# Kernel optimization log

Hardware: AMD Instinct MI355X
Metric: run time of the kernel (lower is better)

Reference implementation:

```python
import jax, jax.numpy as jnp
import numpy as np

LN_EPS = 1e-5


def setup_inputs() -> dict:
    key = jax.random.key(0)
    k1, k2, k3, k4, k5 = jax.random.split(key, 5)
    N, D, E, T = 100000, 128, 400000, 4  # nodes, feat dim, edges per etype, n etypes
    feat = jax.random.normal(k1, (N, D), dtype=jnp.float32)
    W = jax.random.normal(k2, (T, D, D), dtype=jnp.float32)
    Wf = jax.random.normal(k3, (T, D, 2 * D), dtype=jnp.float32)
    ln_w = jnp.ones((D,), dtype=jnp.float32)
    ln_b = jnp.zeros((D,), dtype=jnp.float32)
    src = jax.random.randint(k4, (T, E), 0, N, dtype=jnp.int32)
    dst = jax.random.randint(k5, (T, E), 0, N, dtype=jnp.int32)
    return {"feat": feat, "W": W, "Wf": Wf, "ln_w": ln_w, "ln_b": ln_b, "src": src, "dst": dst}


def reference(feat, W, Wf, ln_w, ln_b, src, dst):
    N, D = feat.shape
    T = W.shape[0]
    h = jnp.zeros((N, D), dtype=feat.dtype)
    for t in range(T):  # small fixed loop over edge types (structurally distinct weights)
        msg = feat @ W[t]                    # [N, D] per-src-node projection
        fw = feat @ Wf[t]                    # [N, 2D] FiLM params (dst ntype == src ntype)
        gamma, beta = fw[:, :D], fw[:, D:]
        m = jax.nn.relu(gamma * msg + beta)  # node-wise FiLM + ReLU, pre-scatter
        # copy_u -> gather message at edge src; fn.sum -> segment-sum into dst
        h = h + jax.ops.segment_sum(m[src[t]], dst[t], num_segments=N)
    # LayerNorm (elementwise affine); dropout omitted (eval mode)
    mu = jnp.mean(h, axis=-1, keepdims=True)
    var = jnp.mean(jnp.square(h - mu), axis=-1, keepdims=True)
    out = (h - mu) * jax.lax.rsqrt(var + LN_EPS) * ln_w + ln_b
    return out
```

## Files before the change

### kernel.cpp

```cpp
#include <hip/hip_runtime.h>
#include <hip/hip_bf16.h>

#define DD 128
#define LN_EPS 1e-5f
#define BCAP 3072
#define MAXBIN 1024
#define CHUNK 4096

typedef __bf16 bf16x8 __attribute__((ext_vector_type(8)));
typedef float f32x4 __attribute__((ext_vector_type(4)));

__device__ __forceinline__ float bflo(unsigned int u) { return __uint_as_float(u << 16); }
__device__ __forceinline__ float bfhi(unsigned int u) { return __uint_as_float(u & 0xffff0000u); }

__device__ __forceinline__ void gload_lds16(const void* g, void* lds) {
    __builtin_amdgcn_global_load_lds(
        (const __attribute__((address_space(1))) unsigned int*)g,
        (__attribute__((address_space(3))) unsigned int*)lds, 16, 0, 0);
}

__global__ __launch_bounds__(256) void k_pack_feat(const float* __restrict__ f,
                                                   unsigned short* __restrict__ fb, int n8) {
    int i = blockIdx.x * 256 + threadIdx.x;
    if (i >= n8) return;
    const float4* p = (const float4*)f + (size_t)i * 2;
    float4 v0 = p[0], v1 = p[1];
    float vv[8] = {v0.x, v0.y, v0.z, v0.w, v1.x, v1.y, v1.z, v1.w};
    unsigned short u[8];
#pragma unroll
    for (int j = 0; j < 8; j++) {
        __hip_bfloat16 b = __float2bfloat16(vv[j]);
        u[j] = *reinterpret_cast<unsigned short*>(&b);
    }
    uint4 o;
    o.x = u[0] | ((unsigned)u[1] << 16);
    o.y = u[2] | ((unsigned)u[3] << 16);
    o.z = u[4] | ((unsigned)u[5] << 16);
    o.w = u[6] | ((unsigned)u[7] << 16);
    ((uint4*)fb)[i] = o;
}

__global__ __launch_bounds__(256) void k_pack_w(const float* __restrict__ W,
                                                const float* __restrict__ Wf,
                                                unsigned short* __restrict__ wcat) {
    int i = blockIdx.x * 256 + threadIdx.x;
    if (i >= 4 * 384 * 128) return;
    int t = i / (384 * 128);
    int r = i % (384 * 128);
    int c = r / 128, k = r % 128;
    float v = (c < 128) ? W[((size_t)t * 128 + k) * 128 + c]
                        : Wf[((size_t)t * 128 + k) * 256 + (c - 128)];
    __hip_bfloat16 b = __float2bfloat16(v);
    wcat[i] = *reinterpret_cast<unsigned short*>(&b);
}

__global__ __launch_bounds__(256) void k_hist2(const int* __restrict__ dst,
                                               int* __restrict__ H, int E4, int NBLK, int NBIN) {
    __shared__ int h[MAXBIN];
    const int b = blockIdx.x;
    for (int j = threadIdx.x; j < NBIN; j += 256) h[j] = 0;
    __syncthreads();
    int base = b * CHUNK;
    int end = base + CHUNK < E4 ? base + CHUNK : E4;
    for (int i = base + threadIdx.x; i < end; i += 256) atomicAdd(&h[dst[i] >> 7], 1);
    __syncthreads();
    for (int j = threadIdx.x; j < NBIN; j += 256) H[(size_t)j * NBLK + b] = h[j];
}

__global__ __launch_bounds__(256) void k_scanbin(int* __restrict__ H, int* __restrict__ C,
                                                 int NBLK, int NBIN) {
    const int wv = (blockIdx.x * 256 + threadIdx.x) >> 6;
    const int lane = threadIdx.x & 63;
    if (wv >= NBIN) return;
    int* row = H + (size_t)wv * NBLK;
    int run = 0;
    for (int base = 0; base < NBLK; base += 64) {
        int idx = base + lane;
        int v = (idx < NBLK) ? row[idx] : 0;
        int s = v;
#pragma unroll
        for (int o = 1; o < 64; o <<= 1) {
            int u = __shfl_up(s, o, 64);
            if (lane >= o) s += u;
        }
        if (idx < NBLK) row[idx] = run + s - v;
        run += __shfl(s, 63, 64);
    }
    if (lane == 0) C[wv] = run;
}

__global__ __launch_bounds__(1024) void k_scan(const int* __restrict__ cnt,
                                               int* __restrict__ off, int NB) {
    __shared__ int s[1024];
    int tid = threadIdx.x;
    s[tid] = (tid < NB) ? cnt[tid] : 0;
    __syncthreads();
    for (int st = 1; st < 1024; st <<= 1) {
        int t = s[tid];
        int a = (tid >= st) ? s[tid - st] : 0;
        __syncthreads();
        s[tid] = t + a;
        __syncthreads();
    }
    if (tid < NB) {
        off[tid] = s[tid] - cnt[tid];
        if (tid == NB - 1) off[NB] = s[tid];
    }
}

__global__ __launch_bounds__(256) void k_place2(const int* __restrict__ src,
                                                const int* __restrict__ dst,
                                                const int* __restrict__ H,
                                                const int* __restrict__ binoff,
                                                unsigned int* __restrict__ rec,
                                                int N, int E, int E4, int NBLK, int NBIN) {
    __shared__ int fill[MAXBIN];
    const int b = blockIdx.x;
    for (int j = threadIdx.x; j < NBIN; j += 256)
        fill[j] = binoff[j] + H[(size_t)j * NBLK + b];
    __syncthreads();
    int base = b * CHUNK;
    int end = base + CHUNK < E4 ? base + CHUNK : E4;
    for (int i = base + threadIdx.x; i < end; i += 256) {
        int d = dst[i];
        int t = i / E;
        unsigned int r = ((unsigned)(d & 127) << 19) | (unsigned)(t * N + src[i]);
        int pos = atomicAdd(&fill[d >> 7], 1);
        rec[pos] = r;
    }
}

__global__ __launch_bounds__(256) void k_sortout(const unsigned int* __restrict__ rec,
                                                 const int* __restrict__ binoff,
                                                 unsigned int* __restrict__ sortedg,
                                                 int* __restrict__ nodestart,
                                                 int* __restrict__ nodedeg, int N) {
    __shared__ int lcnt[128], soff[128], sfill[128], tmp[128];
    __shared__ unsigned int sorted[BCAP];
    const int b = blockIdx.x, tid = threadIdx.x;
    const int s0 = binoff[b];
    int n = binoff[b + 1] - s0;
    if (n > BCAP) n = BCAP;

    if (tid < 128) lcnt[tid] = 0;
    __syncthreads();
    for (int j = tid; j < n; j += 256) atomicAdd(&lcnt[rec[s0 + j] >> 19], 1);
    __syncthreads();
    if (tid < 128) tmp[tid] = lcnt[tid];
    __syncthreads();
    for (int st = 1; st < 128; st <<= 1) {
        int t = 0, a = 0;
        if (tid < 128) {
            t = tmp[tid];
            a = (tid >= st) ? tmp[tid - st] : 0;
        }
        __syncthreads();
        if (tid < 128) tmp[tid] = t + a;
        __syncthreads();
    }
    if (tid < 128) {
        int ex = tmp[tid] - lcnt[tid];
        soff[tid] = ex;
        sfill[tid] = ex;
    }
    __syncthreads();
    for (int j = tid; j < n; j += 256) {
        unsigned int r = rec[s0 + j];
        int p = atomicAdd(&sfill[r >> 19], 1);
        sorted[p] = r & 0x7FFFFu;
    }
    __syncthreads();
    for (int j = tid; j < n; j += 256) sortedg[s0 + j] = sorted[j];
    if (tid < 128) {
        int node = b * 128 + tid;
        if (node < N) {
            nodestart[node] = s0 + soff[tid];
            nodedeg[node] = lcnt[tid];
        }
    }
}

__global__ __launch_bounds__(256, 2) void k_gemm_film(const unsigned short* __restrict__ featb,
                                                      const unsigned short* __restrict__ wcat,
                                                      unsigned short* __restrict__ m, int N,
                                                      int NT) {
    __shared__ unsigned char smem[2 * 16384];
    const int t = blockIdx.y;
    const int tid = threadIdx.x;
    const int w = tid >> 6, lane = tid & 63;
    const int lr = lane & 15, kg = lane >> 4;
    const int cbase = w * 32;

    const unsigned short* wt = wcat + (size_t)t * 384 * 128;
    bf16x8 B[4][3][2];
#pragma unroll
    for (int kkI = 0; kkI < 4; kkI++)
#pragma unroll
        for (int mat = 0; mat < 3; mat++)
#pragma unroll
            for (int cj = 0; cj < 2; cj++) {
                int col = mat * 128 + cbase + cj * 16 + lr;
                B[kkI][mat][cj] = *(const bf16x8*)(wt + (size_t)col * 128 + kkI * 32 + kg * 8);
            }

    auto stage = [&](int buf, int r0) {
#pragma unroll
        for (int it = 0; it < 4; it++) {
            int row = it * 16 + w * 4 + (lane >> 4);
            int gr = r0 + row;
            if (gr >= N) gr = N - 1;
            int x = ((lane & 15) * 16) ^ ((row & 7) << 4);
            const unsigned char* g = (const unsigned char*)featb + (size_t)gr * 256 + x;
            gload_lds16(g, smem + buf * 16384 + it * 4096 + w * 1024);
        }
    };

    unsigned short* mt = m + (size_t)t * N * DD;
    int buf = 0;
    int tile = blockIdx.x;
    if (tile < NT) stage(0, tile * 64);

    for (; tile < NT; tile += gridDim.x) {
        __syncthreads();
        int nxt = tile + gridDim.x;
        if (nxt < NT) stage(buf ^ 1, nxt * 64);

        const unsigned char* sm = smem + buf * 16384;
        f32x4 acc[4][3][2] = {};
#pragma unroll
        for (int kkI = 0; kkI < 4; kkI++) {
            bf16x8 a[4];
#pragma unroll
            for (int mi = 0; mi < 4; mi++) {
                int row = mi * 16 + lr;
                int kb = kkI * 64 + kg * 16;
                a[mi] = *(const bf16x8*)(sm + row * 256 + (kb ^ ((row & 7) << 4)));
            }
#pragma unroll
            for (int mi = 0; mi < 4; mi++)
#pragma unroll
                for (int mat = 0; mat < 3; mat++)
#pragma unroll
                    for (int cj = 0; cj < 2; cj++)
                        acc[mi][mat][cj] = __builtin_amdgcn_mfma_f32_16x16x32_bf16(
                            a[mi], B[kkI][mat][cj], acc[mi][mat][cj], 0, 0, 0);
        }

        const int r0 = tile * 64;
#pragma unroll
        for (int mi = 0; mi < 4; mi++)
#pragma unroll
            for (int cj = 0; cj < 2; cj++)
#pragma unroll
                for (int r = 0; r < 4; r++) {
                    int row = r0 + mi * 16 + kg * 4 + r;
                    if (row < N) {
                        float v = acc[mi][1][cj][r] * acc[mi][0][cj][r] + acc[mi][2][cj][r];
                        v = fmaxf(v, 0.0f);
                        __hip_bfloat16 b = __float2bfloat16(v);
                        mt[(size_t)row * DD + cbase + cj * 16 + lr] =
                            *reinterpret_cast<unsigned short*>(&b);
                    }
                }
        buf ^= 1;
    }
}

__global__ __launch_bounds__(256) void k_agg_ln(const unsigned int* __restrict__ sortedg,
                                                const int* __restrict__ nodestart,
                                                const int* __restrict__ nodedeg,
                                                const char* __restrict__ mbase,
                                                const float* __restrict__ lnw,
                                                const float* __restrict__ lnb,
                                                float* __restrict__ out, int N) {
    const int wv = threadIdx.x >> 6, lane = threadIdx.x & 63;
    const int node = blockIdx.x * 4 + wv;
    if (node >= N) return;
    const int start = nodestart[node], deg = nodedeg[node];
    const int q = lane >> 4, sl = lane & 15;
    const unsigned soff = (unsigned)sl * 16u;

    float a[8] = {0.f, 0.f, 0.f, 0.f, 0.f, 0.f, 0.f, 0.f};

    int e = 0;
    for (; e + 16 <= deg; e += 16) {
        unsigned r0 = sortedg[start + e + q];
        unsigned r1 = sortedg[start + e + 4 + q];
        unsigned r2 = sortedg[start + e + 8 + q];
        unsigned r3 = sortedg[start + e + 12 + q];
        uint4 p0 = *(const uint4*)(mbase + (r0 * 256u + soff));
        uint4 p1 = *(const uint4*)(mbase + (r1 * 256u + soff));
        uint4 p2 = *(const uint4*)(mbase + (r2 * 256u + soff));
        uint4 p3 = *(const uint4*)(mbase + (r3 * 256u + soff));
        a[0] += bflo(p0.x) + bflo(p1.x) + bflo(p2.x) + bflo(p3.x);
        a[1] += bfhi(p0.x) + bfhi(p1.x) + bfhi(p2.x) + bfhi(p3.x);
        a[2] += bflo(p0.y) + bflo(p1.y) + bflo(p2.y) + bflo(p3.y);
        a[3] += bfhi(p0.y) + bfhi(p1.y) + bfhi(p2.y) + bfhi(p3.y);
        a[4] += bflo(p0.z) + bflo(p1.z) + bflo(p2.z) + bflo(p3.z);
        a[5] += bfhi(p0.z) + bfhi(p1.z) + bfhi(p2.z) + bfhi(p3.z);
        a[6] += bflo(p0.w) + bflo(p1.w) + bflo(p2.w) + bflo(p3.w);
        a[7] += bfhi(p0.w) + bfhi(p1.w) + bfhi(p2.w) + bfhi(p3.w);
    }
    for (; e + 4 <= deg; e += 4) {
        unsigned r0 = sortedg[start + e + q];
        uint4 p0 = *(const uint4*)(mbase + (r0 * 256u + soff));
        a[0] += bflo(p0.x);
        a[1] += bfhi(p0.x);
        a[2] += bflo(p0.y);
        a[3] += bfhi(p0.y);
        a[4] += bflo(p0.z);
        a[5] += bfhi(p0.z);
        a[6] += bflo(p0.w);
        a[7] += bfhi(p0.w);
    }
    if (e < deg) {
        int idx = e + q;
        float w = (idx < deg) ? 1.0f : 0.0f;
        if (idx >= deg) idx = deg - 1;
        unsigned r0 = sortedg[start + idx];
        uint4 p0 = *(const uint4*)(mbase + (r0 * 256u + soff));
        a[0] += w * bflo(p0.x);
        a[1] += w * bfhi(p0.x);
        a[2] += w * bflo(p0.y);
        a[3] += w * bfhi(p0.y);
        a[4] += w * bflo(p0.z);
        a[5] += w * bfhi(p0.z);
        a[6] += w * bflo(p0.w);
        a[7] += w * bfhi(p0.w);
    }

#pragma unroll
    for (int j = 0; j < 8; j++) {
        a[j] += __shfl_xor(a[j], 16, 64);
        a[j] += __shfl_xor(a[j], 32, 64);
    }
    float s = 0.f, ss = 0.f;
#pragma unroll
    for (int j = 0; j < 8; j++) {
        s += a[j];
        ss += a[j] * a[j];
    }
#pragma unroll
    for (int o = 1; o < 16; o <<= 1) {
        s += __shfl_xor(s, o, 64);
        ss += __shfl_xor(ss, o, 64);
    }
    float mu = s * (1.0f / 128.0f);
    float var = ss * (1.0f / 128.0f) - mu * mu;
    float rstd = rsqrtf(var + LN_EPS);
    if (q == 0) {
        float4 w0 = ((const float4*)lnw)[sl * 2];
        float4 w1 = ((const float4*)lnw)[sl * 2 + 1];
        float4 b0 = ((const float4*)lnb)[sl * 2];
        float4 b1 = ((const float4*)lnb)[sl * 2 + 1];
        float4 o0, o1;
        o0.x = (a[0] - mu) * rstd * w0.x + b0.x;
        o0.y = (a[1] - mu) * rstd * w0.y + b0.y;
        o0.z = (a[2] - mu) * rstd * w0.z + b0.z;
        o0.w = (a[3] - mu) * rstd * w0.w + b0.w;
        o1.x = (a[4] - mu) * rstd * w1.x + b1.x;
        o1.y = (a[5] - mu) * rstd * w1.y + b1.y;
        o1.z = (a[6] - mu) * rstd * w1.z + b1.z;
        o1.w = (a[7] - mu) * rstd * w1.w + b1.w;
        ((float4*)(out + (size_t)node * DD))[sl * 2] = o0;
        ((float4*)(out + (size_t)node * DD))[sl * 2 + 1] = o1;
    }
}

extern "C" void kernel_launch(void* const* d_in, const int* in_sizes, int n_in,
                              void* d_out, int out_size, void* d_ws, size_t ws_size,
                              hipStream_t stream) {
    const float* feat = (const float*)d_in[0];
    const float* W    = (const float*)d_in[1];
    const float* Wf   = (const float*)d_in[2];
    const float* lnw  = (const float*)d_in[3];
    const float* lnb  = (const float*)d_in[4];
    const int* src    = (const int*)d_in[5];
    const int* dst    = (const int*)d_in[6];
    float* out = (float*)d_out;

    const int N = in_sizes[0] / DD;
    const int E = in_sizes[5] / 4;
    const int E4 = 4 * E;
    const int NB = (N + 127) >> 7;
    const int NBLK = (E4 + CHUNK - 1) / CHUNK;
    const int NT = (N + 63) / 64;

    size_t off = 0;
    char* ws = (char*)d_ws;
    auto alloc = [&](size_t bytes) -> void* {
        void* p = ws + off;
        off += (bytes + 255) & ~(size_t)255;
        return p;
    };
    unsigned short* m     = (unsigned short*)alloc((size_t)4 * N * DD * 2);
    unsigned short* featb = (unsigned short*)alloc((size_t)N * DD * 2);
    unsigned short* wcat  = (unsigned short*)alloc((size_t)4 * 384 * 128 * 2);
    int* H      = (int*)alloc((size_t)NB * NBLK * 4);
    int* C      = (int*)alloc((size_t)NB * 4);
    int* binoff = (int*)alloc((size_t)(NB + 1) * 4);
    unsigned int* rec     = (unsigned int*)alloc((size_t)E4 * 4);
    unsigned int* sortedg = (unsigned int*)alloc((size_t)E4 * 4);
    int* nodestart = (int*)alloc((size_t)N * 4);
    int* nodedeg   = (int*)alloc((size_t)N * 4);
    if (off > ws_size) return;

    int n8 = N * DD / 8;
    k_pack_feat<<<(n8 + 255) / 256, 256, 0, stream>>>(feat, featb, n8);
    k_pack_w<<<(4 * 384 * 128 + 255) / 256, 256, 0, stream>>>(W, Wf, wcat);
    k_hist2<<<NBLK, 256, 0, stream>>>(dst, H, E4, NBLK, NB);
    k_scanbin<<<(NB * 64 + 255) / 256, 256, 0, stream>>>(H, C, NBLK, NB);
    k_scan<<<1, 1024, 0, stream>>>(C, binoff, NB);
    k_place2<<<NBLK, 256, 0, stream>>>(src, dst, H, binoff, rec, N, E, E4, NBLK, NB);
    k_sortout<<<NB, 256, 0, stream>>>(rec, binoff, sortedg, nodestart, nodedeg, N);
    dim3 gg(128, 4);
    k_gemm_film<<<gg, 256, 0, stream>>>(featb, wcat, m, N, NT);
    k_agg_ln<<<(N + 3) / 4, 256, 0, stream>>>(sortedg, nodestart, nodedeg,
                                              (const char*)m, lnw, lnb, out, N);
}
```

Baseline: 173.2 us.

## Fuse preprocessing and bucket-sort kernels into one cooperative kernel with grid syncs

Merges the feature and weight bf16 packing, histogram, bin scan, global scan, placement and per-bin sort into a single cooperative kernel. Grid-wide syncs separate the phases instead of seven separate launches, and the sort phase uses a grid-stride loop over bins. This removes launch overhead and inter-kernel gaps. The risk is that the grid (NBLK of about 391 blocks at 256 threads, 14KB LDS each) must be fully co-resident for the cooperative launch, and grid.sync itself has a cost.

```diff
diff --git a/kernel.cpp b/kernel.cpp
--- a/kernel.cpp
+++ b/kernel.cpp
@@ -1,5 +1,8 @@
 #include <hip/hip_runtime.h>
 #include <hip/hip_bf16.h>
+#include <hip/hip_cooperative_groups.h>
+
+namespace cg = cooperative_groups;
 
 #define DD 128
 #define LN_EPS 1e-5f
@@ -19,163 +22,182 @@
         (__attribute__((address_space(3))) unsigned int*)lds, 16, 0, 0);
 }
 
-__global__ __launch_bounds__(256) void k_pack_feat(const float* __restrict__ f,
-                                                   unsigned short* __restrict__ fb, int n8) {
-    int i = blockIdx.x * 256 + threadIdx.x;
-    if (i >= n8) return;
-    const float4* p = (const float4*)f + (size_t)i * 2;
-    float4 v0 = p[0], v1 = p[1];
-    float vv[8] = {v0.x, v0.y, v0.z, v0.w, v1.x, v1.y, v1.z, v1.w};
-    unsigned short u[8];
-#pragma unroll
-    for (int j = 0; j < 8; j++) {
-        __hip_bfloat16 b = __float2bfloat16(vv[j]);
-        u[j] = *reinterpret_cast<unsigned short*>(&b);
-    }
-    uint4 o;
-    o.x = u[0] | ((unsigned)u[1] << 16);
-    o.y = u[2] | ((unsigned)u[3] << 16);
-    o.z = u[4] | ((unsigned)u[5] << 16);
-    o.w = u[6] | ((unsigned)u[7] << 16);
-    ((uint4*)fb)[i] = o;
-}
-
-__global__ __launch_bounds__(256) void k_pack_w(const float* __restrict__ W,
-                                                const float* __restrict__ Wf,
-                                                unsigned short* __restrict__ wcat) {
-    int i = blockIdx.x * 256 + threadIdx.x;
-    if (i >= 4 * 384 * 128) return;
-    int t = i / (384 * 128);
-    int r = i % (384 * 128);
-    int c = r / 128, k = r % 128;
-    float v = (c < 128) ? W[((size_t)t * 128 + k) * 128 + c]
-                        : Wf[((size_t)t * 128 + k) * 256 + (c - 128)];
-    __hip_bfloat16 b = __float2bfloat16(v);
-    wcat[i] = *reinterpret_cast<unsigned short*>(&b);
-}
-
-__global__ __launch_bounds__(256) void k_hist2(const int* __restrict__ dst,
-                                               int* __restrict__ H, int E4, int NBLK, int NBIN) {
-    __shared__ int h[MAXBIN];
-    const int b = blockIdx.x;
-    for (int j = threadIdx.x; j < NBIN; j += 256) h[j] = 0;
+__global__ __launch_bounds__(256) void k_prep(const float* __restrict__ feat,
+                                              const float* __restrict__ W,
+                                              const float* __restrict__ Wf,
+                                              const int* __restrict__ src,
+                                              const int* __restrict__ dst,
+                                              unsigned short* __restrict__ fb,
+                                              unsigned short* __restrict__ wcat,
+                                              int* __restrict__ H, int* __restrict__ C,
+                                              int* __restrict__ binoff,
+                                              unsigned int* __restrict__ rec,
+                                              unsigned int* __restrict__ sortedg,
+                                              int* __restrict__ nodestart,
+                                              int* __restrict__ nodedeg,
+                                              int N, int E, int E4, int NBLK, int NBIN,
+                                              int n8) {
+    cg::grid_group grid = cg::this_grid();
+    __shared__ int shm[3584];
+    const int b = blockIdx.x, tid = threadIdx.x;
+    const int gtid = b * 256 + tid, gsz = gridDim.x * 256;
+
+    for (int j = tid; j < NBIN; j += 256) shm[j] = 0;
     __syncthreads();
-    int base = b * CHUNK;
-    int end = base + CHUNK < E4 ? base + CHUNK : E4;
-    for (int i = base + threadIdx.x; i < end; i += 256) atomicAdd(&h[dst[i] >> 7], 1);
+    {
+        int base = b * CHUNK;
+        int end = base + CHUNK < E4 ? base + CHUNK : E4;
+        for (int i = base + tid; i < end; i += 256) atomicAdd(&shm[dst[i] >> 7], 1);
+    }
     __syncthreads();
-    for (int j = threadIdx.x; j < NBIN; j += 256) H[(size_t)j * NBLK + b] = h[j];
-}
-
-__global__ __launch_bounds__(256) void k_scanbin(int* __restrict__ H, int* __restrict__ C,
-                                                 int NBLK, int NBIN) {
-    const int wv = (blockIdx.x * 256 + threadIdx.x) >> 6;
-    const int lane = threadIdx.x & 63;
-    if (wv >= NBIN) return;
-    int* row = H + (size_t)wv * NBLK;
-    int run = 0;
-    for (int base = 0; base < NBLK; base += 64) {
-        int idx = base + lane;
-        int v = (idx < NBLK) ? row[idx] : 0;
-        int s = v;
-#pragma unroll
-        for (int o = 1; o < 64; o <<= 1) {
-            int u = __shfl_up(s, o, 64);
-            if (lane >= o) s += u;
-        }
-        if (idx < NBLK) row[idx] = run + s - v;
-        run += __shfl(s, 63, 64);
-    }
-    if (lane == 0) C[wv] = run;
-}
-
-__global__ __launch_bounds__(1024) void k_scan(const int* __restrict__ cnt,
-                                               int* __restrict__ off, int NB) {
-    __shared__ int s[1024];
-    int tid = threadIdx.x;
-    s[tid] = (tid < NB) ? cnt[tid] : 0;
+    for (int j = tid; j < NBIN; j += 256) H[(size_t)j * NBLK + b] = shm[j];
+
+    for (int i = gtid; i < n8; i += gsz) {
+        const float4* p = (const float4*)feat + (size_t)i * 2;
+        float4 v0 = p[0], v1 = p[1];
+        float vv[8] = {v0.x, v0.y, v0.z, v0.w, v1.x, v1.y, v1.z, v1.w};
+        unsigned short u[8];
+#pragma unroll
+        for (int j = 0; j < 8; j++) {
+            __hip_bfloat16 bb = __float2bfloat16(vv[j]);
+            u[j] = *reinterpret_cast<unsigned short*>(&bb);
+        }
+        uint4 o;
+        o.x = u[0] | ((unsigned)u[1] << 16);
+        o.y = u[2] | ((unsigned)u[3] << 16);
+        o.z = u[4] | ((unsigned)u[5] << 16);
+        o.w = u[6] | ((unsigned)u[7] << 16);
+        ((uint4*)fb)[i] = o;
+    }
+
+    for (int i = gtid; i < 4 * 384 * 128; i += gsz) {
+        int t = i / (384 * 128);
+        int r = i % (384 * 128);
+        int c = r / 128, k = r % 128;
+        float v = (c < 128) ? W[((size_t)t * 128 + k) * 128 + c]
+                            : Wf[((size_t)t * 128 + k) * 256 + (c - 128)];
+        __hip_bfloat16 bb = __float2bfloat16(v);
+        wcat[i] = *reinterpret_cast<unsigned short*>(&bb);
+    }
+
+    grid.sync();
+
+    {
+        int wv = gtid >> 6;
+        int lane = tid & 63;
+        if (wv < NBIN) {
+            int* row = H + (size_t)wv * NBLK;
+            int run = 0;
+            for (int base = 0; base < NBLK; base += 64) {
+                int idx = base + lane;
+                int v = (idx < NBLK) ? row[idx] : 0;
+                int s = v;
+#pragma unroll
+                for (int o = 1; o < 64; o <<= 1) {
+                    int u = __shfl_up(s, o, 64);
+                    if (lane >= o) s += u;
+                }
+                if (idx < NBLK) row[idx] = run + s - v;
+                run += __shfl(s, 63, 64);
+            }
+            if (lane == 0) C[wv] = run;
+        }
+    }
+
+    grid.sync();
+
+    if (b == 0) {
+        int v[4];
+        int tot = 0;
+#pragma unroll
+        for (int j = 0; j < 4; j++) {
+            int idx = tid * 4 + j;
+            v[j] = (idx < NBIN) ? C[idx] : 0;
+            tot += v[j];
+        }
+        shm[tid] = tot;
+        __syncthreads();
+        for (int st = 1; st < 256; st <<= 1) {
+            int t = shm[tid];
+            int add = (tid >= st) ? shm[tid - st] : 0;
+            __syncthreads();
+            shm[tid] = t + add;
+            __syncthreads();
+        }
+        int run = shm[tid] - tot;
+#pragma unroll
+        for (int j = 0; j < 4; j++) {
+            int idx = tid * 4 + j;
+            if (idx < NBIN) binoff[idx] = run;
+            run += v[j];
+        }
+        if (tid == 255) binoff[NBIN] = shm[255];
+    }
+
+    grid.sync();
+
+    for (int j = tid; j < NBIN; j += 256) shm[j] = binoff[j] + H[(size_t)j * NBLK + b];
     __syncthreads();
-    for (int st = 1; st < 1024; st <<= 1) {
-        int t = s[tid];
-        int a = (tid >= st) ? s[tid - st] : 0;
-        __syncthreads();
-        s[tid] = t + a;
-        __syncthreads();
-    }
-    if (tid < NB) {
-        off[tid] = s[tid] - cnt[tid];
-        if (tid == NB - 1) off[NB] = s[tid];
-    }
-}
-
-__global__ __launch_bounds__(256) void k_place2(const int* __restrict__ src,
-                                                const int* __restrict__ dst,
-                                                const int* __restrict__ H,
-                                                const int* __restrict__ binoff,
-                                                unsigned int* __restrict__ rec,
-                                                int N, int E, int E4, int NBLK, int NBIN) {
-    __shared__ int fill[MAXBIN];
-    const int b = blockIdx.x;
-    for (int j = threadIdx.x; j < NBIN; j += 256)
-        fill[j] = binoff[j] + H[(size_t)j * NBLK + b];
-    __syncthreads();
-    int base = b * CHUNK;
-    int end = base + CHUNK < E4 ? base + CHUNK : E4;
-    for (int i = base + threadIdx.x; i < end; i += 256) {
-        int d = dst[i];
-        int t = i / E;
-        unsigned int r = ((unsigned)(d & 127) << 19) | (unsigned)(t * N + src[i]);
-        int pos = atomicAdd(&fill[d >> 7], 1);
-        rec[pos] = r;
-    }
-}
-
-__global__ __launch_bounds__(256) void k_sortout(const unsigned int* __restrict__ rec,
-                                                 const int* __restrict__ binoff,
-                                                 unsigned int* __restrict__ sortedg,
-                                                 int* __restrict__ nodestart,
-                                                 int* __restrict__ nodedeg, int N) {
-    __shared__ int lcnt[128], soff[128], sfill[128], tmp[128];
-    __shared__ unsigned int sorted[BCAP];
-    const int b = blockIdx.x, tid = threadIdx.x;
-    const int s0 = binoff[b];
-    int n = binoff[b + 1] - s0;
-    if (n > BCAP) n = BCAP;
-
-    if (tid < 128) lcnt[tid] = 0;
-    __syncthreads();
-    for (int j = tid; j < n; j += 256) atomicAdd(&lcnt[rec[s0 + j] >> 19], 1);
-    __syncthreads();
-    if (tid < 128) tmp[tid] = lcnt[tid];
-    __syncthreads();
-    for (int st = 1; st < 128; st <<= 1) {
-        int t = 0, a = 0;
+    {
+        int base = b * CHUNK;
+        int end = base + CHUNK < E4 ? base + CHUNK : E4;
+        for (int i = base + tid; i < end; i += 256) {
+            int d = dst[i];
+            int t = i / E;
+            unsigned int r = ((unsigned)(d & 127) << 19) | (unsigned)(t * N + src[i]);
+            int pos = atomicAdd(&shm[d >> 7], 1);
+            rec[pos] = r;
+        }
+    }
+
+    grid.sync();
+
+    int* lcnt = shm;
+    int* soff = shm + 128;
+    int* sfill = shm + 256;
+    int* tmp = shm + 384;
+    unsigned int* sorted = (unsigned int*)(shm + 512);
+    for (int bin = b; bin < NBIN; bin += gridDim.x) {
+        __syncthreads();
+        const int s0 = binoff[bin];
+        int n = binoff[bin + 1] - s0;
+        if (n > BCAP) n = BCAP;
+
+        if (tid < 128) lcnt[tid] = 0;
+        __syncthreads();
+        for (int j = tid; j < n; j += 256) atomicAdd(&lcnt[rec[s0 + j] >> 19], 1);
+        __syncthreads();
+        if (tid < 128) tmp[tid] = lcnt[tid];
+        __syncthreads();
+        for (int st = 1; st < 128; st <<= 1) {
+            int t = 0, a = 0;
+            if (tid < 128) {
+                t = tmp[tid];
+                a = (tid >= st) ? tmp[tid - st] : 0;
+            }
+            __syncthreads();
+            if (tid < 128) tmp[tid] = t + a;
+            __syncthreads();
+        }
         if (tid < 128) {
-            t = tmp[tid];
-            a = (tid >= st) ? tmp[tid - st] : 0;
-        }
-        __syncthreads();
-        if (tid < 128) tmp[tid] = t + a;
-        __syncthreads();
-    }
-    if (tid < 128) {
-        int ex = tmp[tid] - lcnt[tid];
-        soff[tid] = ex;
-        sfill[tid] = ex;
-    }
-    __syncthreads();
-    for (int j = tid; j < n; j += 256) {
-        unsigned int r = rec[s0 + j];
-        int p = atomicAdd(&sfill[r >> 19], 1);
-        sorted[p] = r & 0x7FFFFu;
-    }
-    __syncthreads();
-    for (int j = tid; j < n; j += 256) sortedg[s0 + j] = sorted[j];
-    if (tid < 128) {
-        int node = b * 128 + tid;
-        if (node < N) {
-            nodestart[node] = s0 + soff[tid];
-            nodedeg[node] = lcnt[tid];
+            int ex = tmp[tid] - lcnt[tid];
+            soff[tid] = ex;
+            sfill[tid] = ex;
+        }
+        __syncthreads();
+        for (int j = tid; j < n; j += 256) {
+            unsigned int r = rec[s0 + j];
+            int p = atomicAdd(&sfill[r >> 19], 1);
+            sorted[p] = r & 0x7FFFFu;
+        }
+        __syncthreads();
+        for (int j = tid; j < n; j += 256) sortedg[s0 + j] = sorted[j];
+        if (tid < 128) {
+            int node = bin * 128 + tid;
+            if (node < N) {
+                nodestart[node] = s0 + soff[tid];
+                nodedeg[node] = lcnt[tid];
+            }
         }
     }
 }
@@ -257,9 +279,9 @@
                     if (row < N) {
                         float v = acc[mi][1][cj][r] * acc[mi][0][cj][r] + acc[mi][2][cj][r];
                         v = fmaxf(v, 0.0f);
-                        __hip_bfloat16 b = __float2bfloat16(v);
+                        __hip_bfloat16 bb = __float2bfloat16(v);
                         mt[(size_t)row * DD + cbase + cj * 16 + lr] =
-                            *reinterpret_cast<unsigned short*>(&b);
+                            *reinterpret_cast<unsigned short*>(&bb);
                     }
                 }
         buf ^= 1;
@@ -379,12 +401,13 @@
     const int* dst    = (const int*)d_in[6];
     float* out = (float*)d_out;
 
-    const int N = in_sizes[0] / DD;
-    const int E = in_sizes[5] / 4;
-    const int E4 = 4 * E;
-    const int NB = (N + 127) >> 7;
-    const int NBLK = (E4 + CHUNK - 1) / CHUNK;
-    const int NT = (N + 63) / 64;
+    int N = in_sizes[0] / DD;
+    int E = in_sizes[5] / 4;
+    int E4 = 4 * E;
+    int NB = (N + 127) >> 7;
+    int NBLK = (E4 + CHUNK - 1) / CHUNK;
+    int NT = (N + 63) / 64;
+    int n8 = N * DD / 8;
 
     size_t off = 0;
     char* ws = (char*)d_ws;
@@ -405,14 +428,14 @@
     int* nodedeg   = (int*)alloc((size_t)N * 4);
     if (off > ws_size) return;
 
-    int n8 = N * DD / 8;
-    k_pack_feat<<<(n8 + 255) / 256, 256, 0, stream>>>(feat, featb, n8);
-    k_pack_w<<<(4 * 384 * 128 + 255) / 256, 256, 0, stream>>>(W, Wf, wcat);
-    k_hist2<<<NBLK, 256, 0, stream>>>(dst, H, E4, NBLK, NB);
-    k_scanbin<<<(NB * 64 + 255) / 256, 256, 0, stream>>>(H, C, NBLK, NB);
-    k_scan<<<1, 1024, 0, stream>>>(C, binoff, NB);
-    k_place2<<<NBLK, 256, 0, stream>>>(src, dst, H, binoff, rec, N, E, E4, NBLK, NB);
-    k_sortout<<<NB, 256, 0, stream>>>(rec, binoff, sortedg, nodestart, nodedeg, N);
+    {
+        void* args[] = {(void*)&feat, (void*)&W, (void*)&Wf, (void*)&src, (void*)&dst,
+                        (void*)&featb, (void*)&wcat, (void*)&H, (void*)&C, (void*)&binoff,
+                        (void*)&rec, (void*)&sortedg, (void*)&nodestart, (void*)&nodedeg,
+                        (void*)&N, (void*)&E, (void*)&E4, (void*)&NBLK, (void*)&NB,
+                        (void*)&n8};
+        hipLaunchCooperativeKernel((void*)k_prep, dim3(NBLK), dim3(256), args, 0, stream);
+    }
     dim3 gg(128, 4);
     k_gemm_film<<<gg, 256, 0, stream>>>(featb, wcat, m, N, NT);
     k_agg_ln<<<(N + 3) / 4, 256, 0, stream>>>(sortedg, nodestart, nodedeg,
```

Result: slower. 371.2 us (+114.4%).
